# Optimization experiments

Hardware: AMD Instinct MI355X
Metric: run time of the kernel (lower is better)

The kernel has to match this reference:

```python
import jax, jax.numpy as jnp
import numpy as np

# Dims: N batch, I input channels, C = in/hidden/attention/projection/out channels (all 128),
# streams=1, groups=1, spatial kernel 3, dropout 0.
N, I, C, H, W = 8, 128, 128, 36, 36


def _conv(x, w, pad):
    # x: [N, Cin, H, W], w: [Cout, Cin, kh, kw]
    return jax.lax.conv_general_dilated(
        x, w, (1, 1), pad, dimension_numbers=("NCHW", "OIHW", "NCHW"))


def _bias(b):
    return b[None, :, None, None]


def setup_inputs() -> dict:
    key = jax.random.key(0)
    ks = jax.random.split(key, 16)
    std = 0.05

    def w(k, o, i, s):
        return jax.random.normal(k, (o, i, s, s), jnp.float32) * std

    p = {}
    p["inp"] = jax.random.normal(ks[0], (N, I, H, W), jnp.float32)
    p["c0"] = jax.random.normal(ks[1], (1, C, 1, 1), jnp.float32)
    # proj_x: 1x1 conv input->in_channels, bias init 0
    p["w_x"] = w(ks[2], C, I, 1)
    p["b_x"] = jnp.zeros((C,), jnp.float32)
    # token convs (3x3, no bias); q uses SAME pad, k/v VALID
    p["w_qx"] = w(ks[3], C, C, 3)
    p["w_qc"] = w(ks[4], C, C, 3)
    scale = C ** (-0.5)  # gain = attn_channels^-0.5 on k projections
    p["w_kx"] = w(ks[5], C, C, 3) * scale
    p["w_kc"] = w(ks[6], C, C, 3) * scale
    p["w_vx"] = w(ks[7], C, C, 3)
    p["w_vc"] = w(ks[8], C, C, 3)
    # gating 1x1 convs: proj_z (bias=init_gate=1), proj_n (bias=0), in 2*proj channels
    p["w_z"] = w(ks[9], C, 2 * C, 1)
    p["b_z"] = jnp.ones((C,), jnp.float32)
    p["w_n"] = w(ks[10], C, 2 * C, 1)
    p["b_n"] = jnp.zeros((C,), jnp.float32)
    # proj_h: in_channels + 2*projection_channels -> hidden
    p["w_h"] = w(ks[11], C, 3 * C, 1)
    p["b_h"] = jnp.zeros((C,), jnp.float32)
    # output 1x1 conv hidden -> out_channels
    p["w_o"] = w(ks[12], C, C, 1)
    p["b_o"] = jnp.zeros((C,), jnp.float32)
    return p


def reference(inp, c0, w_x, b_x, w_qx, w_qc, w_kx, w_kc, w_vx, w_vc,
              w_z, b_z, w_n, b_n, w_h, b_h, w_o, b_o):
    # proj_x (1x1) -> x: [N, C, H, W]
    x = _conv(inp, w_x, "VALID") + _bias(b_x)
    n_, _, hh, ww = x.shape
    c = jnp.broadcast_to(c0, (n_, c0.shape[1], hh, ww))
    q_len = hh * ww
    # q: SAME pad -> Q = H*W tokens; k/v: VALID -> D = (H-2)*(W-2) tokens
    q = jnp.stack([_conv(x, w_qx, "SAME"), _conv(c, w_qc, "SAME")], 0)
    q = q.reshape(2, n_, -1, q_len)                      # [A, N, C, Q]
    k_x = _conv(x, w_kx, "VALID")
    d_len = k_x.shape[2] * k_x.shape[3]
    k = jnp.stack([k_x, _conv(c, w_kc, "VALID")], 0).reshape(2, n_, -1, d_len)   # [B, N, C, D]
    v = jnp.stack([_conv(x, w_vx, "VALID"), _conv(c, w_vc, "VALID")], 0)
    v = v.reshape(2, n_, -1, d_len)                      # [B, N, C, D]
    # all (A query source) x (B key/value source) attention pairs
    attn = jax.nn.softmax(jnp.einsum("ancq,bncd->anbqd", q, k), axis=-1)
    a = jnp.einsum("bncd,anbqd->anbcq", v, attn)         # [A, N, B, C, Q]
    a = a.reshape(2, n_, -1, hh, ww)                     # channels = B*C = 2*proj
    a_x, a_c = a[0], a[1]
    # GRU-style gated cell update (stored state; not part of the returned output)
    z = jax.nn.sigmoid(_conv(a_c, w_z, "VALID") + _bias(b_z))
    n_cand = jnp.tanh(_conv(a_c, w_n, "VALID") + _bias(b_n))
    c_new = z * c + (1.0 - z) * n_cand  # noqa: F841 (past['c'] in the original)
    # hidden: tanh(proj_h(cat[x, a_x])), dropout p=0 is identity
    xa = jnp.concatenate([x, a_x], axis=1)               # [N, 3*C, H, W]
    h = jnp.tanh(_conv(xa, w_h, "VALID") + _bias(b_h))
    return _conv(h, w_o, "VALID") + _bias(b_o)           # [N, C, H, W]
```

## Files before the change

### kernel.cpp

```cpp
#include <hip/hip_runtime.h>
#include <hip/hip_bf16.h>
#include <math.h>

#define NN 8
#define CH 128
#define HH 36
#define WWI 36
#define PP 1296
#define DD 1156
#define VP 1280
#define KC 1152
#define QT 81
#define DT 5

typedef __attribute__((ext_vector_type(8))) short short8;
typedef __attribute__((ext_vector_type(4))) float f32x4;

__device__ inline unsigned short f2bf(float f) {
    __hip_bfloat16 h = __float2bfloat16(f);
    return __builtin_bit_cast(unsigned short, h);
}
__device__ inline float fast_tanh(float x) {
    float e = __expf(2.f * x);
    return 1.f - 2.f / (e + 1.f);
}
#define MFMA(a, b, c) __builtin_amdgcn_mfma_f32_16x16x32_bf16((a), (b), (c), 0, 0, 0)

__global__ void k_setup(const float* __restrict__ wq, const float* __restrict__ wk,
                        const float* __restrict__ wv, const float* __restrict__ wh,
                        const float* __restrict__ wo, const float* __restrict__ wx,
                        const float* __restrict__ c0, const float* __restrict__ w_vc,
                        const float* __restrict__ b_h,
                        unsigned short* __restrict__ wcat, unsigned short* __restrict__ whb,
                        unsigned short* __restrict__ wob, unsigned short* __restrict__ wxb,
                        float* __restrict__ hconst)
{
    if (blockIdx.x == 576) {
        __shared__ float c0s[CH];
        __shared__ float part[256];
        __shared__ float vcs[CH];
        const int t = threadIdx.x;
        const int c = t & 127, half = t >> 7;
        if (t < CH) c0s[t] = c0[t];
        __syncthreads();
        {
            const float* row = w_vc + (size_t)c * 1152 + half * 576;
            float s = 0.f;
#pragma unroll 4
            for (int j4 = 0; j4 < 144; ++j4) {
                float4 v = ((const float4*)row)[j4];
                int j = half * 576 + j4 * 4;
                s += v.x * c0s[j / 9] + v.y * c0s[(j + 1) / 9]
                   + v.z * c0s[(j + 2) / 9] + v.w * c0s[(j + 3) / 9];
            }
            part[t] = s;
        }
        __syncthreads();
        if (t < CH) vcs[t] = part[t] + part[t + 128];
        __syncthreads();
        {
            const float* wrow = wh + (size_t)c * 384 + 256 + half * 64;
            float hs = 0.f;
#pragma unroll
            for (int j4 = 0; j4 < 16; ++j4) {
                float4 v = ((const float4*)wrow)[j4];
                int ci = half * 64 + j4 * 4;
                hs += v.x * vcs[ci] + v.y * vcs[ci + 1] + v.z * vcs[ci + 2] + v.w * vcs[ci + 3];
            }
            part[t] = hs;
        }
        __syncthreads();
        if (t < CH) hconst[t] = b_h[t] + part[t] + part[t + 128];
        return;
    }
    int t = blockIdx.x * 256 + threadIdx.x;
    int co = t / KC;
    int rem = t - co * KC;
    int tap = rem >> 7, ci = rem & 127;
    int iidx = co * KC + ci * 9 + tap;
    wcat[t] = f2bf(wq[iidx]);
    wcat[147456 + t] = f2bf(wk[iidx]);
    wcat[294912 + t] = f2bf(wv[iidx]);
    if (t < 32768) {
        int c2 = t >> 8, k2 = t & 255;
        whb[t] = f2bf(wh[c2 * 384 + k2]);
    }
    if (t < 16384) { wob[t] = f2bf(wo[t]); wxb[t] = f2bf(wx[t]); }
}

__global__ __launch_bounds__(64)
void k_proj(const float* __restrict__ inp, const unsigned short* __restrict__ wxb,
            const float* __restrict__ bx, unsigned short* __restrict__ xt)
{
    const int lane = threadIdx.x;
    const int quad = lane >> 4, lrow = lane & 15;
    const int p0 = blockIdx.x * 16;
    const int co0 = blockIdx.y * 64;
    const int n = blockIdx.z;
    const float* in_n = inp + (size_t)n * CH * PP;
    f32x4 acc[4] = {};

#pragma unroll
    for (int ks = 0; ks < 4; ++ks) {
        union { short8 v; unsigned short u[8]; } a;
        int ci0 = ks * 32 + quad * 8;
#pragma unroll
        for (int j = 0; j < 8; ++j)
            a.u[j] = f2bf(in_n[(size_t)(ci0 + j) * PP + p0 + lrow]);
#pragma unroll
        for (int ni = 0; ni < 4; ++ni) {
            short8 b = *(const short8*)&wxb[(size_t)(co0 + ni * 16 + lrow) * CH + ks * 32 + quad * 8];
            acc[ni] = MFMA(a.v, b, acc[ni]);
        }
    }
    unsigned short* xn = xt + (size_t)n * PP * CH;
#pragma unroll
    for (int ni = 0; ni < 4; ++ni) {
        float bv = bx[co0 + ni * 16 + lrow];
#pragma unroll
        for (int r = 0; r < 4; ++r)
            xn[(size_t)(p0 + quad * 4 + r) * CH + co0 + ni * 16 + lrow] = f2bf(acc[ni][r] + bv);
    }
}

__global__ __launch_bounds__(256)
void k_conv(const unsigned short* __restrict__ xt, const unsigned short* __restrict__ wcat,
            unsigned short* __restrict__ qt, unsigned short* __restrict__ kt,
            unsigned short* __restrict__ vb)
{
    __shared__ unsigned short lA[2][64 * 72];
    const int t = threadIdx.x;
    const int wave = t >> 6, lane = t & 63;
    const int quad = lane >> 4, lrow = lane & 15;
    const int mode = blockIdx.y;
    const int n = blockIdx.z;
    const int limit = (mode == 0) ? PP : DD;
    const int tile0 = blockIdx.x * 64;
    if (tile0 >= limit) return;
    const unsigned short* xn = xt + (size_t)n * PP * CH;
    const unsigned short* wb = wcat + (size_t)mode * 128 * KC;

    const int arow = t >> 2, aseg = t & 3;
    int apr, apc;
    {
        int tok = tile0 + arow; if (tok >= limit) tok = limit - 1;
        int dv = (mode == 0) ? 36 : 34;
        apr = tok / dv; apc = tok - apr * dv;
    }
    const unsigned short* wr0 = wb + (size_t)((wave * 2 + 0) * 16 + lrow) * KC;
    const unsigned short* wr1 = wb + (size_t)((wave * 2 + 1) * 16 + lrow) * KC;

    uint4 ra0, ra1;
    auto loadA = [&](int ks) {
        int tap = ks >> 1;
        int ky = tap / 3, kx = tap - ky * 3;
        int ci = (ks & 1) * 64 + aseg * 16;
        if (mode == 0) {
            int yy = apr + ky - 1, xx = apc + kx - 1;
            bool ok = (yy >= 0) && (yy < HH) && (xx >= 0) && (xx < WWI);
            ra0 = make_uint4(0, 0, 0, 0);
            ra1 = make_uint4(0, 0, 0, 0);
            if (ok) {
                const unsigned short* p = &xn[(size_t)(yy * WWI + xx) * CH + ci];
                ra0 = *(const uint4*)p;
                ra1 = *(const uint4*)(p + 8);
            }
        } else {
            int yy = apr + ky, xx = apc + kx;
            const unsigned short* p = &xn[(size_t)(yy * WWI + xx) * CH + ci];
            ra0 = *(const uint4*)p;
            ra1 = *(const uint4*)(p + 8);
        }
    };
    auto storeA = [&](int buf) {
        *(uint4*)&lA[buf][arow * 72 + aseg * 16] = ra0;
        *(uint4*)&lA[buf][arow * 72 + aseg * 16 + 8] = ra1;
    };

    short8 b0[2], b1[2], n0[2], n1[2];
    auto loadB = [&](int ks, short8* d0, short8* d1) {
        int off = (ks >> 1) * 128 + (ks & 1) * 64 + quad * 8;
        d0[0] = *(const short8*)(wr0 + off);
        d0[1] = *(const short8*)(wr0 + off + 32);
        d1[0] = *(const short8*)(wr1 + off);
        d1[1] = *(const short8*)(wr1 + off + 32);
    };

    f32x4 acc[4][2] = {};
    loadA(0);
    storeA(0);
    loadB(0, b0, b1);
    __syncthreads();

#pragma unroll
    for (int ks = 0; ks < 18; ++ks) {
        const int buf = ks & 1;
        if (ks < 17) {
            loadA(ks + 1);
            loadB(ks + 1, n0, n1);
        }
#pragma unroll
        for (int sub = 0; sub < 2; ++sub)
#pragma unroll
            for (int mi = 0; mi < 4; ++mi) {
                short8 a = *(const short8*)&lA[buf][(mi * 16 + lrow) * 72 + sub * 32 + quad * 8];
                acc[mi][0] = MFMA(a, b0[sub], acc[mi][0]);
                acc[mi][1] = MFMA(a, b1[sub], acc[mi][1]);
            }
        if (ks < 17) {
            storeA(buf ^ 1);
            b0[0] = n0[0]; b0[1] = n0[1];
            b1[0] = n1[0]; b1[1] = n1[1];
        }
        __syncthreads();
    }

    if (mode == 0) {
        unsigned short* qn = qt + (size_t)n * PP * CH;
#pragma unroll
        for (int mi = 0; mi < 4; ++mi)
#pragma unroll
            for (int r = 0; r < 4; ++r) {
                int p = tile0 + mi * 16 + quad * 4 + r;
                if (p < PP)
#pragma unroll
                    for (int ni = 0; ni < 2; ++ni)
                        qn[(size_t)p * CH + (wave * 2 + ni) * 16 + lrow] = f2bf(acc[mi][ni][r]);
            }
    } else if (mode == 1) {
        unsigned short* kn = kt + (size_t)n * DD * CH;
#pragma unroll
        for (int mi = 0; mi < 4; ++mi)
#pragma unroll
            for (int r = 0; r < 4; ++r) {
                int d = tile0 + mi * 16 + quad * 4 + r;
                if (d < DD)
#pragma unroll
                    for (int ni = 0; ni < 2; ++ni)
                        kn[(size_t)d * CH + (wave * 2 + ni) * 16 + lrow] = f2bf(acc[mi][ni][r]);
            }
    } else {
        unsigned short* vn = vb + (size_t)n * CH * VP;
#pragma unroll
        for (int mi = 0; mi < 4; ++mi)
#pragma unroll
            for (int r = 0; r < 4; ++r) {
                int d = tile0 + mi * 16 + quad * 4 + r;
                if (d < DD)
#pragma unroll
                    for (int ni = 0; ni < 2; ++ni)
                        vn[(size_t)((wave * 2 + ni) * 16 + lrow) * VP + d] = f2bf(acc[mi][ni][r]);
            }
    }
}

__global__ __launch_bounds__(256)
void k_attn(const unsigned short* __restrict__ qt, const unsigned short* __restrict__ kt,
            const unsigned short* __restrict__ vb, _Float16* __restrict__ po,
            float* __restrict__ pm, float* __restrict__ pl)
{
    __shared__ unsigned short lbuf[128 * 136];
    __shared__ unsigned short lp[4][16 * 136];
    const int t = threadIdx.x;
    const int wave = t >> 6, lane = t & 63;
    const int quad = lane >> 4, lrow = lane & 15;
    const int qg = blockIdx.x;
    const int dt = blockIdx.y;
    const int n = blockIdx.z;
    const int qti = qg * 4 + wave;
    const int d0 = dt * 256;
    const unsigned short* qn = qt + (size_t)n * PP * CH;
    const unsigned short* kn = kt + (size_t)n * DD * CH;
    const unsigned short* vn = vb + (size_t)n * CH * VP;

    const int srow = t >> 1;
    const int scol = (t & 1) * 64;
    const int sdst = srow * 136 + scol;

    short8 qa[4];
    {
        int qrow = qti * 16 + lrow; if (qrow >= PP) qrow = PP - 1;
#pragma unroll
        for (int ks = 0; ks < 4; ++ks)
            qa[ks] = *(const short8*)&qn[(size_t)qrow * CH + ks * 32 + quad * 8];
    }

    f32x4 o[8] = {};
    float mx[4] = {-1e30f, -1e30f, -1e30f, -1e30f};
    float rs[4] = {0.f, 0.f, 0.f, 0.f};

#pragma unroll
    for (int h = 0; h < 2; ++h) {
        const int dbase = d0 + h * 128;

        {
            int krow = dbase + srow; if (krow >= DD) krow = DD - 1;
            const unsigned short* src = kn + (size_t)krow * CH + scol;
#pragma unroll
            for (int j = 0; j < 8; ++j)
                *(uint4*)&lbuf[sdst + j * 8] = *(const uint4*)(src + j * 8);
        }
        __syncthreads();

        f32x4 s[8] = {};
        __builtin_amdgcn_s_setprio(1);
#pragma unroll
        for (int ks = 0; ks < 4; ++ks)
#pragma unroll
            for (int ni = 0; ni < 8; ++ni) {
                short8 b = *(const short8*)&lbuf[(ni * 16 + lrow) * 136 + ks * 32 + quad * 8];
                s[ni] = MFMA(qa[ks], b, s[ni]);
            }
        __builtin_amdgcn_s_setprio(0);
        __syncthreads();

        {
            const unsigned short* src = vn + (size_t)srow * VP + dbase + scol;
#pragma unroll
            for (int j = 0; j < 8; ++j)
                *(uint4*)&lbuf[sdst + j * 8] = *(const uint4*)(src + j * 8);
        }

#pragma unroll
        for (int ni = 0; ni < 8; ++ni)
            if (dbase + ni * 16 + lrow >= DD)
#pragma unroll
                for (int r = 0; r < 4; ++r) s[ni][r] = -1e30f;

        float hm[4] = {-1e30f, -1e30f, -1e30f, -1e30f};
#pragma unroll
        for (int ni = 0; ni < 8; ++ni)
#pragma unroll
            for (int r = 0; r < 4; ++r) hm[r] = fmaxf(hm[r], s[ni][r]);
#pragma unroll
        for (int off = 1; off < 16; off <<= 1)
#pragma unroll
            for (int r = 0; r < 4; ++r) hm[r] = fmaxf(hm[r], __shfl_xor(hm[r], off, 64));

        float m[4], sc[4];
#pragma unroll
        for (int r = 0; r < 4; ++r) {
            m[r] = fmaxf(mx[r], hm[r]);
            sc[r] = __expf(mx[r] - m[r]);
        }

        float hs[4] = {0.f, 0.f, 0.f, 0.f};
#pragma unroll
        for (int ni = 0; ni < 8; ++ni)
#pragma unroll
            for (int r = 0; r < 4; ++r) {
                float e = __expf(s[ni][r] - m[r]);
                s[ni][r] = e;
                hs[r] += e;
            }
#pragma unroll
        for (int off = 1; off < 16; off <<= 1)
#pragma unroll
            for (int r = 0; r < 4; ++r) hs[r] += __shfl_xor(hs[r], off, 64);
#pragma unroll
        for (int r = 0; r < 4; ++r) {
            rs[r] = rs[r] * sc[r] + hs[r];
            mx[r] = m[r];
        }
#pragma unroll
        for (int ni = 0; ni < 8; ++ni)
#pragma unroll
            for (int r = 0; r < 4; ++r) o[ni][r] *= sc[r];

#pragma unroll
        for (int ni = 0; ni < 8; ++ni)
#pragma unroll
            for (int r = 0; r < 4; ++r)
                lp[wave][(quad * 4 + r) * 136 + ni * 16 + lrow] = f2bf(s[ni][r]);

        __syncthreads();

        __builtin_amdgcn_s_setprio(1);
#pragma unroll
        for (int kd = 0; kd < 4; ++kd) {
            short8 pa = *(const short8*)&lp[wave][lrow * 136 + kd * 32 + quad * 8];
#pragma unroll
            for (int ni = 0; ni < 8; ++ni) {
                short8 b = *(const short8*)&lbuf[(ni * 16 + lrow) * 136 + kd * 32 + quad * 8];
                o[ni] = MFMA(pa, b, o[ni]);
            }
        }
        __builtin_amdgcn_s_setprio(0);
        if (h == 0) __syncthreads();
    }

    if (qti < QT) {
        const int base = (n * QT + qti) * DT + dt;
        _Float16* pob = po + (size_t)base * 2048;
#pragma unroll
        for (int ni = 0; ni < 8; ++ni)
#pragma unroll
            for (int r = 0; r < 4; ++r)
                pob[(quad * 4 + r) * 128 + ni * 16 + lrow] = (_Float16)o[ni][r];
        if (lrow == 0)
#pragma unroll
            for (int r = 0; r < 4; ++r) {
                pm[base * 16 + quad * 4 + r] = mx[r];
                pl[base * 16 + quad * 4 + r] = rs[r];
            }
    }
}

__global__ __launch_bounds__(256)
void k_ahout(const _Float16* __restrict__ po, const float* __restrict__ pm,
             const float* __restrict__ pl, const unsigned short* __restrict__ xt,
             const unsigned short* __restrict__ whb, const float* __restrict__ hconst,
             const unsigned short* __restrict__ wob, const float* __restrict__ bo,
             float* __restrict__ out)
{
    __shared__ float sm[80], ssc[80], smg[16], sli[16];
    __shared__ unsigned short la0[16 * 136];
    __shared__ unsigned short lh[16 * 136];
    const int qti = blockIdx.x;
    const int n = blockIdx.y;
    const int base = (n * QT + qti) * DT;
    const int t = threadIdx.x;

    if (t < 80) sm[t] = pm[base * 16 + t];
    __syncthreads();
    if (t < 16) {
        float mg = -1e30f;
#pragma unroll
        for (int dt = 0; dt < DT; ++dt) mg = fmaxf(mg, sm[dt * 16 + t]);
        float ls = 0.f;
#pragma unroll
        for (int dt = 0; dt < DT; ++dt) ls += __expf(sm[dt * 16 + t] - mg) * pl[base * 16 + dt * 16 + t];
        smg[t] = mg; sli[t] = 1.f / ls;
    }
    __syncthreads();
    if (t < 80) ssc[t] = __expf(sm[t] - smg[t & 15]);
    __syncthreads();
#pragma unroll
    for (int k = 0; k < 8; ++k) {
        int idx = t + k * 256;
        int row = idx >> 7, c = idx & 127;
        float acc = 0.f;
#pragma unroll
        for (int dt = 0; dt < DT; ++dt)
            acc += ssc[dt * 16 + row] * (float)po[(size_t)(base + dt) * 2048 + idx];
        la0[row * 136 + c] = f2bf(acc * sli[row]);
    }
    __syncthreads();

    const int wave = t >> 6, lane = t & 63;
    const int quad = lane >> 4, lrow = lane & 15;
    const int p0 = qti * 16;
    const unsigned short* x0 = xt + (size_t)n * PP * CH;

    f32x4 acc1[2] = {};
#pragma unroll
    for (int ks = 0; ks < 8; ++ks) {
        int col = (ks & 3) * 32 + quad * 8;
        short8 a;
        if (ks < 4) a = *(const short8*)&x0[(size_t)(p0 + lrow) * CH + col];
        else        a = *(const short8*)&la0[lrow * 136 + col];
#pragma unroll
        for (int j = 0; j < 2; ++j) {
            int ni = wave * 2 + j;
            short8 b = *(const short8*)&whb[(size_t)(ni * 16 + lrow) * 256 + ks * 32 + quad * 8];
            acc1[j] = MFMA(a, b, acc1[j]);
        }
    }
#pragma unroll
    for (int j = 0; j < 2; ++j) {
        int ni = wave * 2 + j;
        float hc = hconst[ni * 16 + lrow];
#pragma unroll
        for (int r = 0; r < 4; ++r)
            lh[(quad * 4 + r) * 136 + ni * 16 + lrow] = f2bf(fast_tanh(acc1[j][r] + hc));
    }
    __syncthreads();

    f32x4 acc2[2] = {};
#pragma unroll
    for (int ks = 0; ks < 4; ++ks) {
        short8 a = *(const short8*)&lh[lrow * 136 + ks * 32 + quad * 8];
#pragma unroll
        for (int j = 0; j < 2; ++j) {
            int ni = wave * 2 + j;
            short8 b = *(const short8*)&wob[(size_t)(ni * 16 + lrow) * CH + ks * 32 + quad * 8];
            acc2[j] = MFMA(a, b, acc2[j]);
        }
    }
#pragma unroll
    for (int j = 0; j < 2; ++j) {
        int ni = wave * 2 + j;
        float bv = bo[ni * 16 + lrow];
#pragma unroll
        for (int r = 0; r < 4; ++r)
            out[((size_t)(n * CH + ni * 16 + lrow)) * PP + p0 + quad * 4 + r] = acc2[j][r] + bv;
    }
}

extern "C" void kernel_launch(void* const* d_in, const int* in_sizes, int n_in,
                              void* d_out, int out_size, void* d_ws, size_t ws_size,
                              hipStream_t stream)
{
    const float* inp  = (const float*)d_in[0];
    const float* c0   = (const float*)d_in[1];
    const float* w_x  = (const float*)d_in[2];
    const float* b_x  = (const float*)d_in[3];
    const float* w_qx = (const float*)d_in[4];
    const float* w_kx = (const float*)d_in[6];
    const float* w_vx = (const float*)d_in[8];
    const float* w_vc = (const float*)d_in[9];
    const float* w_h  = (const float*)d_in[14];
    const float* b_h  = (const float*)d_in[15];
    const float* w_o  = (const float*)d_in[16];
    const float* b_o  = (const float*)d_in[17];
    float* out = (float*)d_out;

    char* w = (char*)d_ws;
    unsigned short* xt   = (unsigned short*)(w);
    unsigned short* qt   = (unsigned short*)(w + 2654208);
    unsigned short* kt   = (unsigned short*)(w + 5308416);
    unsigned short* vb   = (unsigned short*)(w + 7675904);
    unsigned short* wcat = (unsigned short*)(w + 12951552);
    unsigned short* wxb  = (unsigned short*)(w + 13836288);
    unsigned short* whb  = (unsigned short*)(w + 13869056);
    unsigned short* wob  = (unsigned short*)(w + 13934592);
    float* hconst        = (float*)(w + 13967360);
    float* pm            = (float*)(w + 13967872);
    float* pl            = (float*)(w + 14382592);
    _Float16* po         = (_Float16*)(w + 14797312);

    hipLaunchKernelGGL(k_setup, dim3(577), dim3(256), 0, stream,
                       w_qx, w_kx, w_vx, w_h, w_o, w_x, c0, w_vc, b_h,
                       wcat, whb, wob, wxb, hconst);

    hipLaunchKernelGGL(k_proj, dim3(QT, 2, NN), dim3(64), 0, stream, inp, wxb, b_x, xt);

    hipLaunchKernelGGL(k_conv, dim3(21, 3, NN), dim3(256), 0, stream, xt, wcat, qt, kt, vb);

    hipLaunchKernelGGL(k_attn, dim3(21, DT, NN), dim3(256), 0, stream, qt, kt, vb, po, pm, pl);

    hipLaunchKernelGGL(k_ahout, dim3(QT, NN), dim3(256), 0, stream,
                       po, pm, pl, xt, whb, hconst, wob, b_o, out);
}
```

Before: 208.9 us.

## Load K/V MFMA operands directly from global memory instead of shared LDS staging

Removes the shared K/V staging buffer and block-wide barriers in the attention kernel. Each wave now reads its K and V MFMA B-operands straight from global memory, relying on L1/L2 since the four waves share the same tiles. A wave-local waitcnt plus sched barrier replaces the block sync around the P buffer. Occupancy is hinted at 3 blocks per CU. The trade is fewer barriers and less LDS against redundant, less coalesced global loads per wave.

```diff
diff --git a/kernel.cpp b/kernel.cpp
--- a/kernel.cpp
+++ b/kernel.cpp
@@ -254,12 +254,11 @@
     }
 }
 
-__global__ __launch_bounds__(256)
+__global__ __launch_bounds__(256, 3)
 void k_attn(const unsigned short* __restrict__ qt, const unsigned short* __restrict__ kt,
             const unsigned short* __restrict__ vb, _Float16* __restrict__ po,
             float* __restrict__ pm, float* __restrict__ pl)
 {
-    __shared__ unsigned short lbuf[128 * 136];
     __shared__ unsigned short lp[4][16 * 136];
     const int t = threadIdx.x;
     const int wave = t >> 6, lane = t & 63;
@@ -273,10 +272,6 @@
     const unsigned short* kn = kt + (size_t)n * DD * CH;
     const unsigned short* vn = vb + (size_t)n * CH * VP;
 
-    const int srow = t >> 1;
-    const int scol = (t & 1) * 64;
-    const int sdst = srow * 136 + scol;
-
     short8 qa[4];
     {
         int qrow = qti * 16 + lrow; if (qrow >= PP) qrow = PP - 1;
@@ -293,33 +288,15 @@
     for (int h = 0; h < 2; ++h) {
         const int dbase = d0 + h * 128;
 
-        {
-            int krow = dbase + srow; if (krow >= DD) krow = DD - 1;
-            const unsigned short* src = kn + (size_t)krow * CH + scol;
-#pragma unroll
-            for (int j = 0; j < 8; ++j)
-                *(uint4*)&lbuf[sdst + j * 8] = *(const uint4*)(src + j * 8);
-        }
-        __syncthreads();
-
         f32x4 s[8] = {};
-        __builtin_amdgcn_s_setprio(1);
 #pragma unroll
         for (int ks = 0; ks < 4; ++ks)
 #pragma unroll
             for (int ni = 0; ni < 8; ++ni) {
-                short8 b = *(const short8*)&lbuf[(ni * 16 + lrow) * 136 + ks * 32 + quad * 8];
+                int kr = dbase + ni * 16 + lrow; if (kr >= DD) kr = DD - 1;
+                short8 b = *(const short8*)&kn[(size_t)kr * CH + ks * 32 + quad * 8];
                 s[ni] = MFMA(qa[ks], b, s[ni]);
             }
-        __builtin_amdgcn_s_setprio(0);
-        __syncthreads();
-
-        {
-            const unsigned short* src = vn + (size_t)srow * VP + dbase + scol;
-#pragma unroll
-            for (int j = 0; j < 8; ++j)
-                *(uint4*)&lbuf[sdst + j * 8] = *(const uint4*)(src + j * 8);
-        }
 
 #pragma unroll
         for (int ni = 0; ni < 8; ++ni)
@@ -372,21 +349,18 @@
 #pragma unroll
             for (int r = 0; r < 4; ++r)
                 lp[wave][(quad * 4 + r) * 136 + ni * 16 + lrow] = f2bf(s[ni][r]);
-
-        __syncthreads();
-
-        __builtin_amdgcn_s_setprio(1);
+        asm volatile("s_waitcnt lgkmcnt(0)" ::: "memory");
+        __builtin_amdgcn_sched_barrier(0);
+
 #pragma unroll
         for (int kd = 0; kd < 4; ++kd) {
             short8 pa = *(const short8*)&lp[wave][lrow * 136 + kd * 32 + quad * 8];
 #pragma unroll
             for (int ni = 0; ni < 8; ++ni) {
-                short8 b = *(const short8*)&lbuf[(ni * 16 + lrow) * 136 + kd * 32 + quad * 8];
+                short8 b = *(const short8*)&vn[(size_t)(ni * 16 + lrow) * VP + dbase + kd * 32 + quad * 8];
                 o[ni] = MFMA(pa, b, o[ni]);
             }
         }
-        __builtin_amdgcn_s_setprio(0);
-        if (h == 0) __syncthreads();
     }
 
     if (qti < QT) {
```

Result: slower. 229.4 us (+9.8%).
